# Optimization experiments

Measured on AMD Instinct MI355X. Metric: run time of the kernel, lower is better.

The kernel has to match this reference:

```python
import jax, jax.numpy as jnp
import numpy as np
from math import sqrt

# Dims: B batch, L frames, N points/frame, DIM transformer dim,
# J joints, M memory slots per joint, FD final_dim = DIM//8, OUT = 3*J
B, L, N, DIM = 4, 24, 512, 1024
J, M, FD, OUT = 24, 64, 128, 72


def setup_inputs() -> dict:
    key = jax.random.key(0)
    ks = jax.random.split(key, 8)
    w = lambda k, shape: jax.random.normal(k, shape, jnp.float32) * 0.02
    return {
        "feat": jax.random.normal(ks[0], (B, L, N, DIM), jnp.float32),
        "seg_w": w(ks[1], (J, DIM)),
        "seg_b": jnp.zeros((J,), jnp.float32),
        "pc_w": w(ks[2], (FD, DIM)),
        "pc_b": jnp.zeros((FD,), jnp.float32),
        "mem": jax.random.normal(ks[3], (FD, J * M), jnp.float32),
        "ln_g": jnp.ones((FD,), jnp.float32),
        "ln_b": jnp.zeros((FD,), jnp.float32),
        "w1": w(ks[4], (FD // 2, FD)),
        "b1": jnp.zeros((FD // 2,), jnp.float32),
        "w2": w(ks[5], (OUT, FD // 2)),
        "b2": jnp.zeros((OUT,), jnp.float32),
    }


def forward_mem(y, s, mem):
    # y: (B, Nt, D) point features; s: (B, Nt, J) seg weights; mem: (D, J*M)
    Bn, Nt, D = y.shape
    # affinity of every token to every (joint, slot) memory entry
    logits = jnp.einsum('dk,bnd->bkn', mem, y) / sqrt(D)            # (B, J*M, Nt)
    # per-joint segmentation weighting of the logits
    logits = logits.reshape(Bn, J, M, Nt) * s.transpose(0, 2, 1)[:, :, None, :]
    attn = jax.nn.softmax(logits.reshape(Bn, J * M, Nt), axis=1)     # over memory slots
    return jnp.einsum('dk,bkn->bnd', mem, attn)                      # (B, Nt, D)


def reference(feat, seg_w, seg_b, pc_w, pc_b, mem, ln_g, ln_b, w1, b1, w2, b2):
    Bn, Lf, Np, C = feat.shape
    # seg_head: 1x1 conv == per-point linear -> softmax over joints
    seg = jnp.einsum('blnc,jc->blnj', feat, seg_w) + seg_b           # (B,L,N,J)
    seg = jax.nn.softmax(seg.reshape(Bn, Lf * Np, J), axis=-1)       # (B, L*N, J)
    seg_out = seg.reshape(Bn, Lf, Np, J).transpose(0, 1, 3, 2)       # (B,L,J,N)
    # pc_head: per-point projection to final_dim
    pc = (jnp.einsum('blnc,fc->blnf', feat, pc_w) + pc_b).reshape(Bn, Lf * Np, FD)
    rec = forward_mem(pc, seg, mem)                                  # (B, L*N, FD)
    loss_rec = jnp.mean((rec - pc) ** 2)
    skl = jnp.max(rec, axis=1)                                       # (B, FD)
    # skl_head: LayerNorm -> Linear -> GELU -> Linear
    mu = jnp.mean(skl, axis=-1, keepdims=True)
    var = jnp.var(skl, axis=-1, keepdims=True)
    h = (skl - mu) * jax.lax.rsqrt(var + 1e-5) * ln_g + ln_b
    h = jax.nn.gelu(h @ w1.T + b1, approximate=False)
    skl_out = h @ w2.T + b2                                          # (B, OUT)
    return skl_out, seg_out, loss_rec
```

## Files before the change

kernel.cpp:

```cpp
#include <hip/hip_runtime.h>

typedef __bf16 bf16_t;
typedef bf16_t bf16x8 __attribute__((ext_vector_type(8)));
typedef float f32x4 __attribute__((ext_vector_type(4)));
typedef unsigned short u16;

#define MFMA16 __builtin_amdgcn_mfma_f32_16x16x32_bf16

#define NT_TOK   12288
#define T_TOK    49152

#define WS_PC    0
#define WS_S     25165824
#define WS_WP    29884416
#define WS_MTP   30212096
#define WS_MFP   30605312
#define WS_SKL   30998528
#define WS_LOSS  31000576

__device__ __forceinline__ u16 f2bf(float f) {
  union { bf16_t h; u16 u; } c; c.h = (bf16_t)f; return c.u;
}

__device__ __forceinline__ void atomic_max_f32(float* a, float v) {
  if (v >= 0.f) atomicMax((int*)a, __float_as_int(v));
  else atomicMin((unsigned int*)a, (unsigned int)__float_as_int(v));
}

#define GLD16(g, l) __builtin_amdgcn_global_load_lds( \
    (const __attribute__((address_space(1))) void*)(g), \
    (__attribute__((address_space(3))) void*)(l), 16, 0, 0)

__global__ void k_init(const float* __restrict__ seg_w, const float* __restrict__ pc_w,
                       const float* __restrict__ mem,
                       u16* __restrict__ Wp, u16* __restrict__ mTp, u16* __restrict__ mFp,
                       float* __restrict__ skl, float* __restrict__ loss)
{
  int i = blockIdx.x * 256 + threadIdx.x;
  union { u16 s[8]; uint4 v; } u;
  if (i < 20480) {
    int lane = i & 63, blk = i >> 6;
    int kc = blk / 10, t = blk - kc * 10;
    int n = lane & 15, q = lane >> 4;
    int row = t * 16 + n;
    int k0 = kc * 32 + q * 8;
    #pragma unroll
    for (int e = 0; e < 8; ++e) {
      float v = 0.f;
      if (row < 24) v = seg_w[row * 1024 + k0 + e];
      else if (row < 152) v = pc_w[(row - 24) * 1024 + k0 + e];
      u.s[e] = f2bf(v);
    }
    *(uint4*)(Wp + (size_t)i * 8) = u.v;
  } else if ((i -= 20480) < 24576) {
    int lane = i & 63, blk = i >> 6;
    int j = blk >> 4, rem = blk & 15, wv = rem >> 2, ks = rem & 3;
    int n = lane & 15, q = lane >> 4;
    int slot = j * 64 + wv * 16 + n;
    int d0 = ks * 32 + q * 8;
    #pragma unroll
    for (int e = 0; e < 8; ++e)
      u.s[e] = f2bf(mem[(size_t)(d0 + e) * 1536 + slot]);
    *(uint4*)(mTp + (size_t)i * 8) = u.v;
  } else if ((i -= 24576) < 24576) {
    int lane = i & 63, blk = i >> 6;
    int j = blk >> 4, h = (blk >> 3) & 1, wv = (blk >> 1) & 3, ft = blk & 1;
    int n = lane & 15, q = lane >> 4;
    int f = wv * 32 + ft * 16 + n;
    int s0 = j * 64 + h * 32 + q * 8;
    #pragma unroll
    for (int e = 0; e < 8; ++e)
      u.s[e] = f2bf(mem[(size_t)f * 1536 + s0 + e]);
    *(uint4*)(mFp + (size_t)i * 8) = u.v;
  } else if ((i -= 24576) < 512) {
    skl[i] = -__builtin_inff();
  } else if (i == 512) {
    *loss = 0.f;
  }
}

__global__ __launch_bounds__(256, 3) void k_proj(
    const float* __restrict__ feat, const u16* __restrict__ Wp,
    const float* __restrict__ seg_b, const float* __restrict__ pc_b,
    float* __restrict__ pc_out, float* __restrict__ s_out, float* __restrict__ out_seg)
{
  __shared__ __align__(16) u16 wbuf[2][10240];

  const int tid = threadIdx.x;
  const int w = tid >> 6;
  const int lane = tid & 63;
  const int n = lane & 15;
  const int q = lane >> 4;
  const int base = blockIdx.x * 64;

  f32x4 acc[10];
  #pragma unroll
  for (int t = 0; t < 10; ++t) acc[t] = (f32x4){0.f, 0.f, 0.f, 0.f};

  const float* fp0 = feat + (size_t)(base + w * 16 + n) * 1024 + q * 8;

  #pragma unroll
  for (int i = 0; i < 5; ++i) {
    const int off = i * 2048 + w * 512;
    GLD16(Wp + off + lane * 8, &wbuf[0][off]);
  }
  __builtin_amdgcn_sched_barrier(0);
  float4 fb[3][2][2];
  #pragma unroll
  for (int cc = 0; cc < 2; ++cc)
    #pragma unroll
    for (int kc2 = 0; kc2 < 2; ++kc2) {
      const float4* a = (const float4*)(fp0 + (cc * 2 + kc2) * 32);
      fb[cc][kc2][0] = a[0];
      fb[cc][kc2][1] = a[1];
    }
  asm volatile("s_waitcnt vmcnt(8)");
  __builtin_amdgcn_s_barrier();
  __builtin_amdgcn_sched_barrier(0);

  #pragma unroll
  for (int c = 0; c < 16; ++c) {
    if (c < 15) {
      const u16* gW = Wp + (size_t)(c + 1) * 10240;
      u16* nb = &wbuf[(c + 1) & 1][0];
      #pragma unroll
      for (int i = 0; i < 5; ++i) {
        const int off = i * 2048 + w * 512;
        GLD16(gW + off + lane * 8, nb + off);
      }
      __builtin_amdgcn_sched_barrier(0);
    }
    if (c < 14) {
      #pragma unroll
      for (int kc2 = 0; kc2 < 2; ++kc2) {
        const float4* a = (const float4*)(fp0 + ((c + 2) * 2 + kc2) * 32);
        fb[(c + 2) % 3][kc2][0] = a[0];
        fb[(c + 2) % 3][kc2][1] = a[1];
      }
    }

    const u16* lb = &wbuf[c & 1][0];
    #pragma unroll
    for (int kc2 = 0; kc2 < 2; ++kc2) {
      bf16x8 bw[10];
      #pragma unroll
      for (int t = 0; t < 10; ++t)
        bw[t] = *(const bf16x8*)(lb + (size_t)(kc2 * 10 + t) * 512 + lane * 8);
      float4 x0 = fb[c % 3][kc2][0], y0 = fb[c % 3][kc2][1];
      bf16x8 af;
      af[0] = (bf16_t)x0.x; af[1] = (bf16_t)x0.y; af[2] = (bf16_t)x0.z; af[3] = (bf16_t)x0.w;
      af[4] = (bf16_t)y0.x; af[5] = (bf16_t)y0.y; af[6] = (bf16_t)y0.z; af[7] = (bf16_t)y0.w;
      #pragma unroll
      for (int t = 0; t < 10; ++t)
        acc[t] = MFMA16(af, bw[t], acc[t], 0, 0, 0);
    }

    if (c < 15) {
      if (c < 14) asm volatile("s_waitcnt vmcnt(4)");
      else        asm volatile("s_waitcnt vmcnt(0)");
      __builtin_amdgcn_s_barrier();
      __builtin_amdgcn_sched_barrier(0);
    }
  }

  #pragma unroll
  for (int r = 0; r < 4; ++r) {
    const int token = base + w * 16 + q * 4 + r;
    float v0 = acc[0][r] + seg_b[n];
    float v1 = (n < 8) ? (acc[1][r] + seg_b[16 + n]) : -__builtin_inff();
    float mx = fmaxf(v0, v1);
    #pragma unroll
    for (int d2 = 1; d2 < 16; d2 <<= 1) mx = fmaxf(mx, __shfl_xor(mx, d2, 16));
    float e0 = __expf(v0 - mx);
    float e1 = (n < 8) ? __expf(v1 - mx) : 0.f;
    float sm = e0 + e1;
    #pragma unroll
    for (int d2 = 1; d2 < 16; d2 <<= 1) sm += __shfl_xor(sm, d2, 16);
    float is = 1.f / sm;
    float s0v = e0 * is, s1v = e1 * is;
    s_out[(size_t)token * 24 + n] = s0v;
    if (n < 8) s_out[(size_t)token * 24 + 16 + n] = s1v;
    const int b = token / NT_TOK;
    const int rem = token - b * NT_TOK;
    const int l = rem >> 9, p = rem & 511;
    float* so = out_seg + ((size_t)(b * 24 + l) * 24) * 512 + p;
    so[(size_t)n * 512] = s0v;
    if (n < 8) so[(size_t)(16 + n) * 512] = s1v;
    #pragma unroll
    for (int t = 1; t < 10; ++t) {
      int col = t * 16 + n;
      if (col >= 24 && col < 152) {
        pc_out[(size_t)token * 128 + (col - 24)] = acc[t][r] + pc_b[col - 24];
      }
    }
  }
}

#define AS_S     0
#define AS_P     6656
#define AS_LW    15872
#define AS_RL    16896
#define AS_TOT   16912

__global__ __launch_bounds__(256, 3) void k_attn(
    const float* __restrict__ pc, const float* __restrict__ s_in,
    const u16* __restrict__ mFp, const u16* __restrict__ mTp,
    float* __restrict__ skl, float* __restrict__ loss)
{
  __shared__ __align__(16) char smem[AS_TOT];
  float* s_tile = (float*)(smem + AS_S);
  u16* Pl  = (u16*)(smem + AS_P);
  float* lw  = (float*)(smem + AS_LW);
  float* redL = (float*)(smem + AS_RL);

  const int tid = threadIdx.x;
  const int w = tid >> 6, lane = tid & 63, n = lane & 15, q = lane >> 4;
  const int base = blockIdx.x * 64;

  for (int i = tid; i < 1536; i += 256) {
    int t = i / 24, jj = i - t * 24;
    s_tile[t * 26 + jj] = s_in[(size_t)base * 24 + i];
  }

  bf16x8 qf[4][4];
  #pragma unroll
  for (int tt = 0; tt < 4; ++tt)
    #pragma unroll
    for (int ks = 0; ks < 4; ++ks) {
      const float4* qp = (const float4*)(pc + (size_t)(base + tt * 16 + n) * 128 + ks * 32 + q * 8);
      float4 x = qp[0], y = qp[1];
      bf16x8 a;
      a[0] = (bf16_t)x.x; a[1] = (bf16_t)x.y; a[2] = (bf16_t)x.z; a[3] = (bf16_t)x.w;
      a[4] = (bf16_t)y.x; a[5] = (bf16_t)y.y; a[6] = (bf16_t)y.z; a[7] = (bf16_t)y.w;
      qf[tt][ks] = a;
    }

  f32x4 o[4][2];
  #pragma unroll
  for (int tt = 0; tt < 4; ++tt) {
    o[tt][0] = (f32x4){0.f, 0.f, 0.f, 0.f};
    o[tt][1] = (f32x4){0.f, 0.f, 0.f, 0.f};
  }
  float l_acc[4] = {0.f, 0.f, 0.f, 0.f};

  const u16* mT_frag = mTp + (size_t)(w * 4) * 512 + lane * 8;
  const u16* mF_frag = mFp + (size_t)(w * 2) * 512 + lane * 8;

  const float invs = 0.088388347648318447f;

  bf16x8 amc[4];
  #pragma unroll
  for (int ks = 0; ks < 4; ++ks)
    amc[ks] = *(const bf16x8*)(mT_frag + (size_t)ks * 512);

  __syncthreads();

  for (int j = 0; j < 24; ++j) {
    bf16x8 bm[4];
    #pragma unroll
    for (int hf = 0; hf < 4; ++hf)
      bm[hf] = *(const bf16x8*)(mF_frag + (size_t)(j * 16 + (hf >> 1) * 8 + (hf & 1)) * 512);

    f32x4 sacc[4];
    #pragma unroll
    for (int tt = 0; tt < 4; ++tt) sacc[tt] = (f32x4){0.f, 0.f, 0.f, 0.f};
    #pragma unroll
    for (int ks = 0; ks < 4; ++ks) {
      #pragma unroll
      for (int tt = 0; tt < 4; ++tt)
        sacc[tt] = MFMA16(amc[ks], qf[tt][ks], sacc[tt], 0, 0, 0);
    }

    bf16x8 amn[4];
    if (j < 23) {
      #pragma unroll
      for (int ks = 0; ks < 4; ++ks)
        amn[ks] = *(const bf16x8*)(mT_frag + (size_t)((j + 1) * 16 + ks) * 512);
    }

    __syncthreads();
    #pragma unroll
    for (int tt = 0; tt < 4; ++tt) {
      float sj = s_tile[(tt * 16 + n) * 26 + j] * invs;
      float p0 = __expf(sacc[tt][0] * sj);
      float p1 = __expf(sacc[tt][1] * sj);
      float p2 = __expf(sacc[tt][2] * sj);
      float p3 = __expf(sacc[tt][3] * sj);
      l_acc[tt] += (p0 + p1) + (p2 + p3);
      ushort4 pk;
      pk.x = f2bf(p0); pk.y = f2bf(p1); pk.z = f2bf(p2); pk.w = f2bf(p3);
      *(ushort4*)(&Pl[(tt * 16 + n) * 72 + w * 16 + q * 4]) = pk;
    }
    __syncthreads();

    #pragma unroll
    for (int tt = 0; tt < 4; ++tt) {
      bf16x8 pa0 = *(const bf16x8*)(&Pl[(tt * 16 + n) * 72 + q * 8]);
      o[tt][0] = MFMA16(pa0, bm[0], o[tt][0], 0, 0, 0);
      o[tt][1] = MFMA16(pa0, bm[1], o[tt][1], 0, 0, 0);
      bf16x8 pa1 = *(const bf16x8*)(&Pl[(tt * 16 + n) * 72 + 32 + q * 8]);
      o[tt][0] = MFMA16(pa1, bm[2], o[tt][0], 0, 0, 0);
      o[tt][1] = MFMA16(pa1, bm[3], o[tt][1], 0, 0, 0);
    }

    #pragma unroll
    for (int ks = 0; ks < 4; ++ks) amc[ks] = amn[ks];
  }

  #pragma unroll
  for (int tt = 0; tt < 4; ++tt) {
    float v = l_acc[tt];
    v += __shfl_xor(v, 16, 64);
    v += __shfl_xor(v, 32, 64);
    if (q == 0) lw[w * 64 + tt * 16 + n] = v;
  }
  __syncthreads();

  float lsum = 0.f;
  float fmax2[2] = {-__builtin_inff(), -__builtin_inff()};
  #pragma unroll
  for (int tt = 0; tt < 4; ++tt) {
    f32x4 linv;
    #pragma unroll
    for (int r = 0; r < 4; ++r) {
      int tok = tt * 16 + q * 4 + r;
      float lt = lw[tok] + lw[64 + tok] + lw[128 + tok] + lw[192 + tok];
      linv[r] = 1.f / lt;
    }
    #pragma unroll
    for (int ft = 0; ft < 2; ++ft)
      #pragma unroll
      for (int r = 0; r < 4; ++r) {
        const int token = base + tt * 16 + q * 4 + r;
        const int f = w * 32 + ft * 16 + n;
        float rec = o[tt][ft][r] * linv[r];
        float d = rec - pc[(size_t)token * 128 + f];
        lsum += d * d;
        fmax2[ft] = fmaxf(fmax2[ft], rec);
      }
  }
  #pragma unroll
  for (int ft = 0; ft < 2; ++ft) {
    float v = fmax2[ft];
    v = fmaxf(v, __shfl_xor(v, 16, 64));
    v = fmaxf(v, __shfl_xor(v, 32, 64));
    if (q == 0) atomic_max_f32(&skl[(base / NT_TOK) * 128 + w * 32 + ft * 16 + n], v);
  }
  #pragma unroll
  for (int d2 = 1; d2 < 64; d2 <<= 1) lsum += __shfl_xor(lsum, d2, 64);
  if (lane == 0) redL[w] = lsum;
  __syncthreads();
  if (tid == 0) atomicAdd(loss, redL[0] + redL[1] + redL[2] + redL[3]);
}

__global__ void k_head(const float* __restrict__ skl,
                       const float* __restrict__ ln_g, const float* __restrict__ ln_b,
                       const float* __restrict__ w1, const float* __restrict__ b1,
                       const float* __restrict__ w2, const float* __restrict__ b2,
                       const float* __restrict__ loss, float* __restrict__ out)
{
  __shared__ float hbuf[128];
  __shared__ float gbuf[64];
  __shared__ float red[4];
  const int t = threadIdx.x;
  const int ln = t & 63, wv = t >> 6;
  for (int b = 0; b < 4; ++b) {
    float x = skl[b * 128 + t];
    float s1 = x, s2 = x * x;
    #pragma unroll
    for (int d = 1; d < 64; d <<= 1) {
      s1 += __shfl_xor(s1, d, 64);
      s2 += __shfl_xor(s2, d, 64);
    }
    if (ln == 0) { red[wv * 2] = s1; red[wv * 2 + 1] = s2; }
    __syncthreads();
    float mu = (red[0] + red[2]) * (1.f / 128.f);
    float var = (red[1] + red[3]) * (1.f / 128.f) - mu * mu;
    float hn = (x - mu) * rsqrtf(var + 1e-5f) * ln_g[t] + ln_b[t];
    hbuf[t] = hn;
    __syncthreads();
    if (t < 64) {
      float a = b1[t];
      for (int c = 0; c < 128; ++c) a += hbuf[c] * w1[t * 128 + c];
      gbuf[t] = 0.5f * a * (1.f + erff(a * 0.70710678118654752f));
    }
    __syncthreads();
    if (t < 72) {
      float a = b2[t];
      for (int c = 0; c < 64; ++c) a += gbuf[c] * w2[t * 64 + c];
      out[b * 72 + t] = a;
    }
    __syncthreads();
  }
  if (t == 0) out[1179936] = loss[0] * (1.f / 6291456.f);
}

extern "C" void kernel_launch(void* const* d_in, const int* in_sizes, int n_in,
                              void* d_out, int out_size, void* d_ws, size_t ws_size,
                              hipStream_t stream) {
  (void)in_sizes; (void)n_in; (void)out_size; (void)ws_size;
  const float* feat  = (const float*)d_in[0];
  const float* seg_w = (const float*)d_in[1];
  const float* seg_b = (const float*)d_in[2];
  const float* pc_w  = (const float*)d_in[3];
  const float* pc_b  = (const float*)d_in[4];
  const float* mem   = (const float*)d_in[5];
  const float* ln_g  = (const float*)d_in[6];
  const float* ln_b  = (const float*)d_in[7];
  const float* w1    = (const float*)d_in[8];
  const float* b1    = (const float*)d_in[9];
  const float* w2    = (const float*)d_in[10];
  const float* b2    = (const float*)d_in[11];

  char* ws = (char*)d_ws;
  float* pc_buf = (float*)(ws + WS_PC);
  float* s_buf  = (float*)(ws + WS_S);
  u16*   Wp     = (u16*)(ws + WS_WP);
  u16*   mTp    = (u16*)(ws + WS_MTP);
  u16*   mFp    = (u16*)(ws + WS_MFP);
  float* sklb   = (float*)(ws + WS_SKL);
  float* lossb  = (float*)(ws + WS_LOSS);
  float* out    = (float*)d_out;

  k_init<<<275, 256, 0, stream>>>(seg_w, pc_w, mem, Wp, mTp, mFp, sklb, lossb);
  k_proj<<<768, 256, 0, stream>>>(feat, Wp, seg_b, pc_b, pc_buf, s_buf, out + 288);
  k_attn<<<768, 256, 0, stream>>>(pc_buf, s_buf, mFp, mTp, sklb, lossb);
  k_head<<<1, 128, 0, stream>>>(sklb, ln_g, ln_b, w1, b1, w2, b2, lossb, out);
}
```

Baseline: 393.5 us.

## Fuse projection and memory-attention kernels, keeping pc and seg tiles in LDS

```diff
diff --git a/kernel.cpp b/kernel.cpp
--- a/kernel.cpp
+++ b/kernel.cpp
@@ -79,12 +79,26 @@
   }
 }
 
-__global__ __launch_bounds__(256, 3) void k_proj(
+#define FS_PCL   0
+#define FS_PL    33792
+#define FS_LW    43008
+#define FS_RL    44032
+#define FS_ST    44048
+#define FS_TOT   50704
+
+__global__ __launch_bounds__(256, 3) void k_fused(
     const float* __restrict__ feat, const u16* __restrict__ Wp,
     const float* __restrict__ seg_b, const float* __restrict__ pc_b,
-    float* __restrict__ pc_out, float* __restrict__ s_out, float* __restrict__ out_seg)
+    const u16* __restrict__ mFp, const u16* __restrict__ mTp,
+    float* __restrict__ out_seg, float* __restrict__ skl, float* __restrict__ loss)
 {
-  __shared__ __align__(16) u16 wbuf[2][10240];
+  __shared__ __align__(16) char smem[FS_TOT];
+  u16*   wb     = (u16*)smem;
+  float* pc_l   = (float*)(smem + FS_PCL);
+  u16*   Pl     = (u16*)(smem + FS_PL);
+  float* lw     = (float*)(smem + FS_LW);
+  float* redL   = (float*)(smem + FS_RL);
+  float* s_tile = (float*)(smem + FS_ST);
 
   const int tid = threadIdx.x;
   const int w = tid >> 6;
@@ -102,7 +116,7 @@
   #pragma unroll
   for (int i = 0; i < 5; ++i) {
     const int off = i * 2048 + w * 512;
-    GLD16(Wp + off + lane * 8, &wbuf[0][off]);
+    GLD16(Wp + off + lane * 8, wb + off);
   }
   __builtin_amdgcn_sched_barrier(0);
   float4 fb[3][2][2];
@@ -114,7 +128,7 @@
       fb[cc][kc2][0] = a[0];
       fb[cc][kc2][1] = a[1];
     }
-  asm volatile("s_waitcnt vmcnt(8)");
+  asm volatile("s_waitcnt vmcnt(8)" ::: "memory");
   __builtin_amdgcn_s_barrier();
   __builtin_amdgcn_sched_barrier(0);
 
@@ -122,7 +136,7 @@
   for (int c = 0; c < 16; ++c) {
     if (c < 15) {
       const u16* gW = Wp + (size_t)(c + 1) * 10240;
-      u16* nb = &wbuf[(c + 1) & 1][0];
+      u16* nb = wb + ((c + 1) & 1) * 10240;
       #pragma unroll
       for (int i = 0; i < 5; ++i) {
         const int off = i * 2048 + w * 512;
@@ -139,7 +153,7 @@
       }
     }
 
-    const u16* lb = &wbuf[c & 1][0];
+    const u16* lb = wb + (c & 1) * 10240;
     #pragma unroll
     for (int kc2 = 0; kc2 < 2; ++kc2) {
       bf16x8 bw[10];
@@ -156,16 +170,22 @@
     }
 
     if (c < 15) {
-      if (c < 14) asm volatile("s_waitcnt vmcnt(4)");
-      else        asm volatile("s_waitcnt vmcnt(0)");
+      if (c < 14) asm volatile("s_waitcnt vmcnt(4)" ::: "memory");
+      else        asm volatile("s_waitcnt vmcnt(0)" ::: "memory");
       __builtin_amdgcn_s_barrier();
       __builtin_amdgcn_sched_barrier(0);
     }
   }
 
+  asm volatile("s_waitcnt lgkmcnt(0)" ::: "memory");
+  __builtin_amdgcn_sched_barrier(0);
+  __builtin_amdgcn_s_barrier();
+  __builtin_amdgcn_sched_barrier(0);
+
   #pragma unroll
   for (int r = 0; r < 4; ++r) {
-    const int token = base + w * 16 + q * 4 + r;
+    const int tl = w * 16 + q * 4 + r;
+    const int token = base + tl;
     float v0 = acc[0][r] + seg_b[n];
     float v1 = (n < 8) ? (acc[1][r] + seg_b[16 + n]) : -__builtin_inff();
     float mx = fmaxf(v0, v1);
@@ -178,8 +198,8 @@
     for (int d2 = 1; d2 < 16; d2 <<= 1) sm += __shfl_xor(sm, d2, 16);
     float is = 1.f / sm;
     float s0v = e0 * is, s1v = e1 * is;
-    s_out[(size_t)token * 24 + n] = s0v;
-    if (n < 8) s_out[(size_t)token * 24 + 16 + n] = s1v;
+    s_tile[tl * 26 + n] = s0v;
+    if (n < 8) s_tile[tl * 26 + 16 + n] = s1v;
     const int b = token / NT_TOK;
     const int rem = token - b * NT_TOK;
     const int l = rem >> 9, p = rem & 511;
@@ -190,44 +210,30 @@
     for (int t = 1; t < 10; ++t) {
       int col = t * 16 + n;
       if (col >= 24 && col < 152) {
-        pc_out[(size_t)token * 128 + (col - 24)] = acc[t][r] + pc_b[col - 24];
+        pc_l[tl * 132 + (col - 24)] = acc[t][r] + pc_b[col - 24];
       }
     }
   }
-}
-
-#define AS_S     0
-#define AS_P     6656
-#define AS_LW    15872
-#define AS_RL    16896
-#define AS_TOT   16912
-
-__global__ __launch_bounds__(256, 3) void k_attn(
-    const float* __restrict__ pc, const float* __restrict__ s_in,
-    const u16* __restrict__ mFp, const u16* __restrict__ mTp,
-    float* __restrict__ skl, float* __restrict__ loss)
-{
-  __shared__ __align__(16) char smem[AS_TOT];
-  float* s_tile = (float*)(smem + AS_S);
-  u16* Pl  = (u16*)(smem + AS_P);
-  float* lw  = (float*)(smem + AS_LW);
-  float* redL = (float*)(smem + AS_RL);
-
-  const int tid = threadIdx.x;
-  const int w = tid >> 6, lane = tid & 63, n = lane & 15, q = lane >> 4;
-  const int base = blockIdx.x * 64;
-
-  for (int i = tid; i < 1536; i += 256) {
-    int t = i / 24, jj = i - t * 24;
-    s_tile[t * 26 + jj] = s_in[(size_t)base * 24 + i];
-  }
+
+  asm volatile("s_waitcnt lgkmcnt(0)" ::: "memory");
+  __builtin_amdgcn_sched_barrier(0);
+  __builtin_amdgcn_s_barrier();
+  __builtin_amdgcn_sched_barrier(0);
+
+  const u16* mT_frag = mTp + (size_t)(w * 4) * 512 + lane * 8;
+  const u16* mF_frag = mFp + (size_t)(w * 2) * 512 + lane * 8;
+
+  bf16x8 amc[4];
+  #pragma unroll
+  for (int ks = 0; ks < 4; ++ks)
+    amc[ks] = *(const bf16x8*)(mT_frag + (size_t)ks * 512);
 
   bf16x8 qf[4][4];
   #pragma unroll
   for (int tt = 0; tt < 4; ++tt)
     #pragma unroll
     for (int ks = 0; ks < 4; ++ks) {
-      const float4* qp = (const float4*)(pc + (size_t)(base + tt * 16 + n) * 128 + ks * 32 + q * 8);
+      const float4* qp = (const float4*)(pc_l + (size_t)(tt * 16 + n) * 132 + ks * 32 + q * 8);
       float4 x = qp[0], y = qp[1];
       bf16x8 a;
       a[0] = (bf16_t)x.x; a[1] = (bf16_t)x.y; a[2] = (bf16_t)x.z; a[3] = (bf16_t)x.w;
@@ -243,17 +249,7 @@
   }
   float l_acc[4] = {0.f, 0.f, 0.f, 0.f};
 
-  const u16* mT_frag = mTp + (size_t)(w * 4) * 512 + lane * 8;
-  const u16* mF_frag = mFp + (size_t)(w * 2) * 512 + lane * 8;
-
   const float invs = 0.088388347648318447f;
-
-  bf16x8 amc[4];
-  #pragma unroll
-  for (int ks = 0; ks < 4; ++ks)
-    amc[ks] = *(const bf16x8*)(mT_frag + (size_t)ks * 512);
-
-  __syncthreads();
 
   for (int j = 0; j < 24; ++j) {
     bf16x8 bm[4];
@@ -278,7 +274,10 @@
         amn[ks] = *(const bf16x8*)(mT_frag + (size_t)((j + 1) * 16 + ks) * 512);
     }
 
-    __syncthreads();
+    __builtin_amdgcn_sched_barrier(0);
+    __builtin_amdgcn_s_barrier();
+    __builtin_amdgcn_sched_barrier(0);
+
     #pragma unroll
     for (int tt = 0; tt < 4; ++tt) {
       float sj = s_tile[(tt * 16 + n) * 26 + j] * invs;
@@ -291,7 +290,11 @@
       pk.x = f2bf(p0); pk.y = f2bf(p1); pk.z = f2bf(p2); pk.w = f2bf(p3);
       *(ushort4*)(&Pl[(tt * 16 + n) * 72 + w * 16 + q * 4]) = pk;
     }
-    __syncthreads();
+
+    asm volatile("s_waitcnt lgkmcnt(0)" ::: "memory");
+    __builtin_amdgcn_sched_barrier(0);
+    __builtin_amdgcn_s_barrier();
+    __builtin_amdgcn_sched_barrier(0);
 
     #pragma unroll
     for (int tt = 0; tt < 4; ++tt) {
@@ -331,10 +334,10 @@
     for (int ft = 0; ft < 2; ++ft)
       #pragma unroll
       for (int r = 0; r < 4; ++r) {
-        const int token = base + tt * 16 + q * 4 + r;
+        const int tl = tt * 16 + q * 4 + r;
         const int f = w * 32 + ft * 16 + n;
         float rec = o[tt][ft][r] * linv[r];
-        float d = rec - pc[(size_t)token * 128 + f];
+        float d = rec - pc_l[(size_t)tl * 132 + f];
         lsum += d * d;
         fmax2[ft] = fmaxf(fmax2[ft], rec);
       }
@@ -413,8 +416,6 @@
   const float* b2    = (const float*)d_in[11];
 
   char* ws = (char*)d_ws;
-  float* pc_buf = (float*)(ws + WS_PC);
-  float* s_buf  = (float*)(ws + WS_S);
   u16*   Wp     = (u16*)(ws + WS_WP);
   u16*   mTp    = (u16*)(ws + WS_MTP);
   u16*   mFp    = (u16*)(ws + WS_MFP);
@@ -423,7 +424,6 @@
   float* out    = (float*)d_out;
 
   k_init<<<275, 256, 0, stream>>>(seg_w, pc_w, mem, Wp, mTp, mFp, sklb, lossb);
-  k_proj<<<768, 256, 0, stream>>>(feat, Wp, seg_b, pc_b, pc_buf, s_buf, out + 288);
-  k_attn<<<768, 256, 0, stream>>>(pc_buf, s_buf, mFp, mTp, sklb, lossb);
+  k_fused<<<768, 256, 0, stream>>>(feat, Wp, seg_b, pc_b, mFp, mTp, out + 288, sklb, lossb);
   k_head<<<1, 128, 0, stream>>>(sklb, ln_g, ln_b, w1, b1, w2, b2, lossb, out);
 }
```

After: 370.4 us. -5.9%, faster.
